# Kernel optimization log

Hardware: AMD Instinct MI355X
Metric: run time of the kernel (lower is better)

Reference implementation:

```python
import jax, jax.numpy as jnp
import numpy as np

N = 8192
F_IN = 128
F_OUT = 128
BLOCK = 64  # row block for the masked neighbor max-pool (keeps peak mem ~256MB)


def setup_inputs() -> dict:
    key = jax.random.key(0)
    k_in, k_adj, k_w, k_b = jax.random.split(key, 4)
    x = jax.random.normal(k_in, (N, F_IN), dtype=jnp.float32)
    adj = (jax.random.uniform(k_adj, (N, N)) < 0.01).astype(jnp.float32)
    adj = adj.at[jnp.arange(N), jnp.arange(N)].set(1.0)
    stdv = 1.0 / np.sqrt(F_OUT)
    weight = jax.random.uniform(k_w, (F_IN, F_OUT), minval=-stdv, maxval=stdv, dtype=jnp.float32)
    bias = jax.random.uniform(k_b, (F_OUT,), minval=-stdv, maxval=stdv, dtype=jnp.float32)
    return {"input": x, "adj": adj, "weight": weight, "bias": bias}


def _graph_pool(out, adj):
    # For each row i: max over features of out[j] where adj[i, j] != 0.
    # Blocked scan over rows to avoid materializing [N, N, F].
    neg = jnp.asarray(jnp.finfo(out.dtype).min, out.dtype)

    def body(_, adj_blk):  # adj_blk: [BLOCK, N]
        masked = jnp.where(adj_blk[:, :, None] != 0, out[None, :, :], neg)  # [BLOCK, N, F]
        return None, jnp.max(masked, axis=1)

    _, blocks = jax.lax.scan(body, None, adj.reshape(N // BLOCK, BLOCK, N))
    return blocks.reshape(N, out.shape[-1])


def reference(input, adj, weight, bias):
    h = input @ weight                       # [N, F_out]
    out = jnp.maximum(adj @ h + bias, 0.0)   # aggregate + bias + relu
    return _graph_pool(out, adj)             # per-node neighbor max-pool
```

## Files before the change

### kernel.cpp

```cpp
#include <hip/hip_runtime.h>
#include <float.h>

constexpr int N = 8192;
constexpr int F = 128;
constexpr int CAP = 256;

using short8 = __attribute__((ext_vector_type(8))) short;
using float4v = __attribute__((ext_vector_type(4))) float;

static __device__ inline unsigned short f2bf(float f) {
    unsigned u = __float_as_uint(f);
    u += 0x7fffu + ((u >> 16) & 1u);
    return (unsigned short)(u >> 16);
}
static __device__ inline float bf2f(unsigned short s) {
    return __uint_as_float((unsigned)s << 16);
}

constexpr int KP = 136;

__global__ __launch_bounds__(256) void gemm_mfma(const float* __restrict__ x,
                                                 const float* __restrict__ w,
                                                 unsigned short* __restrict__ h) {
    __shared__ unsigned short xs[64][KP];
    __shared__ unsigned short wt[128][KP];

    const int tid = threadIdx.x;
    const int row0 = blockIdx.x * 64;

    {
        const float4* x4 = (const float4*)(x + (size_t)row0 * F);
        #pragma unroll
        for (int i = tid; i < 64 * F / 4; i += 256) {
            const float4 v = x4[i];
            const int r = (i * 4) >> 7, c = (i * 4) & 127;
            xs[r][c + 0] = f2bf(v.x); xs[r][c + 1] = f2bf(v.y);
            xs[r][c + 2] = f2bf(v.z); xs[r][c + 3] = f2bf(v.w);
        }
    }
    {
        const float4* w4 = (const float4*)w;
        #pragma unroll
        for (int i = tid; i < F * F / 4; i += 256) {
            const float4 v = w4[i];
            const int k = (i * 4) >> 7, n = (i * 4) & 127;
            wt[n + 0][k] = f2bf(v.x); wt[n + 1][k] = f2bf(v.y);
            wt[n + 2][k] = f2bf(v.z); wt[n + 3][k] = f2bf(v.w);
        }
    }
    __syncthreads();

    const int lane = tid & 63, wid = tid >> 6;
    const int m = lane & 15, quad = lane >> 4;
    const int m0 = wid * 16;

    float4v acc[8];
    #pragma unroll
    for (int nt = 0; nt < 8; ++nt) acc[nt] = (float4v){0.f, 0.f, 0.f, 0.f};

    #pragma unroll
    for (int k0 = 0; k0 < F; k0 += 32) {
        const short8 a = *(const short8*)&xs[m0 + m][k0 + quad * 8];
        #pragma unroll
        for (int nt = 0; nt < 8; ++nt) {
            const short8 b = *(const short8*)&wt[nt * 16 + m][k0 + quad * 8];
            acc[nt] = __builtin_amdgcn_mfma_f32_16x16x32_bf16(a, b, acc[nt], 0, 0, 0);
        }
    }

    #pragma unroll
    for (int nt = 0; nt < 8; ++nt)
        #pragma unroll
        for (int r = 0; r < 4; ++r) {
            const int row = row0 + m0 + quad * 4 + r;
            const int col = nt * 16 + m;
            h[(size_t)row * F + col] = f2bf(acc[nt][r]);
        }
}

__global__ __launch_bounds__(256) void aggregate_relu_build_csr(
        const float* __restrict__ adj,
        const unsigned short* __restrict__ h,
        const float* __restrict__ bias,
        unsigned short* __restrict__ out2,
        unsigned short* __restrict__ csr_idx,
        int* __restrict__ csr_cnt) {
    __shared__ int idx[CAP];
    __shared__ int cnt;
    __shared__ float partial[F];

    const int tid  = threadIdx.x;
    const int lane = tid & 63;
    const int row  = blockIdx.x;

    if (tid == 0) cnt = 0;
    __syncthreads();

    const float4v* arow = (const float4v*)(adj + (size_t)row * N);
    float4v v[8];
    #pragma unroll
    for (int it = 0; it < 8; ++it) v[it] = __builtin_nontemporal_load(arow + tid + it * 256);

    const unsigned long long lt = (1ull << lane) - 1ull;
    #pragma unroll
    for (int it = 0; it < 8; ++it) {
        const int j4 = 4 * (tid + it * 256);
        const float4v vv = v[it];
        const unsigned long long m0 = __ballot(vv.x != 0.f);
        const unsigned long long m1 = __ballot(vv.y != 0.f);
        const unsigned long long m2 = __ballot(vv.z != 0.f);
        const unsigned long long m3 = __ballot(vv.w != 0.f);
        const int c0 = __popcll(m0), c1 = __popcll(m1),
                  c2 = __popcll(m2), c3 = __popcll(m3);
        const int tot = c0 + c1 + c2 + c3;
        int base = 0;
        if (lane == 0 && tot) base = atomicAdd(&cnt, tot);
        base = __shfl(base, 0, 64);
        if (vv.x != 0.f) idx[base + __popcll(m0 & lt)] = j4 + 0;
        base += c0;
        if (vv.y != 0.f) idx[base + __popcll(m1 & lt)] = j4 + 1;
        base += c1;
        if (vv.z != 0.f) idx[base + __popcll(m2 & lt)] = j4 + 2;
        base += c2;
        if (vv.w != 0.f) idx[base + __popcll(m3 & lt)] = j4 + 3;
    }
    __syncthreads();

    const int n = min(cnt, CAP);

    if (tid == 0) csr_cnt[row] = n;
    if (tid < n) csr_idx[(size_t)row * CAP + tid] = (unsigned short)idx[tid];

    const int f = tid & (F - 1);
    const int half = tid >> 7;

    float acc = 0.f;
    int e = half;
    for (; e + 6 < n; e += 8) {
        const int j0 = idx[e], j1 = idx[e + 2], j2 = idx[e + 4], j3 = idx[e + 6];
        const float a0 = bf2f(h[(size_t)j0 * F + f]);
        const float a1 = bf2f(h[(size_t)j1 * F + f]);
        const float a2 = bf2f(h[(size_t)j2 * F + f]);
        const float a3 = bf2f(h[(size_t)j3 * F + f]);
        acc += (a0 + a1) + (a2 + a3);
    }
    for (; e < n; e += 2) acc += bf2f(h[(size_t)idx[e] * F + f]);

    if (half == 1) partial[f] = acc;
    __syncthreads();
    if (half == 0) {
        acc += partial[f];
        const float vb = acc + bias[f];
        out2[(size_t)row * F + f] = f2bf(vb > 0.f ? vb : 0.f);
    }
}

__global__ __launch_bounds__(256) void neighbor_max_csr(
        const unsigned short* __restrict__ csr_idx,
        const int* __restrict__ csr_cnt,
        const unsigned short* __restrict__ out2,
        float* __restrict__ out) {
    __shared__ int idx[CAP];
    __shared__ float partial[F];

    const int tid = threadIdx.x;
    const int row = blockIdx.x;

    const int n = csr_cnt[row];
    if (tid < n) idx[tid] = csr_idx[(size_t)row * CAP + tid];
    __syncthreads();

    const int f = tid & (F - 1);
    const int half = tid >> 7;

    float acc = -FLT_MAX;
    int e = half;
    for (; e + 6 < n; e += 8) {
        const int j0 = idx[e], j1 = idx[e + 2], j2 = idx[e + 4], j3 = idx[e + 6];
        const float a0 = bf2f(out2[(size_t)j0 * F + f]);
        const float a1 = bf2f(out2[(size_t)j1 * F + f]);
        const float a2 = bf2f(out2[(size_t)j2 * F + f]);
        const float a3 = bf2f(out2[(size_t)j3 * F + f]);
        acc = fmaxf(acc, fmaxf(fmaxf(a0, a1), fmaxf(a2, a3)));
    }
    for (; e < n; e += 2) acc = fmaxf(acc, bf2f(out2[(size_t)idx[e] * F + f]));

    if (half == 1) partial[f] = acc;
    __syncthreads();
    if (half == 0) {
        acc = fmaxf(acc, partial[f]);
        out[(size_t)row * F + f] = acc;
    }
}

extern "C" void kernel_launch(void* const* d_in, const int* in_sizes, int n_in,
                              void* d_out, int out_size, void* d_ws, size_t ws_size,
                              hipStream_t stream) {
    const float* x    = (const float*)d_in[0];
    const float* adj  = (const float*)d_in[1];
    const float* w    = (const float*)d_in[2];
    const float* bias = (const float*)d_in[3];
    float* out = (float*)d_out;

    unsigned short* h    = (unsigned short*)d_ws;
    unsigned short* out2 = h + (size_t)N * F;
    int* csr_cnt = (int*)(out2 + (size_t)N * F);
    unsigned short* csr_idx = (unsigned short*)(csr_cnt + N);

    gemm_mfma<<<N / 64, 256, 0, stream>>>(x, w, h);
    aggregate_relu_build_csr<<<N, 256, 0, stream>>>(adj, h, bias, out2, csr_idx, csr_cnt);
    neighbor_max_csr<<<N, 256, 0, stream>>>(csr_idx, csr_cnt, out2, out);
}
```

Measured before the change: 386.5 us.

## Pack bf16 pairs per lane and split neighbor gathers across four wavefronts

The aggregate and max-pool kernels now have each lane load one 32-bit word holding two bf16 features. Each of the four wavefronts covers a full 128-feature row for every fourth neighbor, then partials are combined through shared memory. This halves the gather load instructions per neighbor and makes bias loads and output stores wider. The GEMM also uses 32-row tiles split into two column halves per wave, doubling the block count and halving accumulator registers, at the cost of reloading W per block. The dominant cost is still streaming the dense adjacency, so overall gains may be limited.

```diff
diff --git a/kernel.cpp b/kernel.cpp
--- a/kernel.cpp
+++ b/kernel.cpp
@@ -22,16 +22,16 @@
 __global__ __launch_bounds__(256) void gemm_mfma(const float* __restrict__ x,
                                                  const float* __restrict__ w,
                                                  unsigned short* __restrict__ h) {
-    __shared__ unsigned short xs[64][KP];
+    __shared__ unsigned short xs[32][KP];
     __shared__ unsigned short wt[128][KP];
 
     const int tid = threadIdx.x;
-    const int row0 = blockIdx.x * 64;
+    const int row0 = blockIdx.x * 32;
 
     {
         const float4* x4 = (const float4*)(x + (size_t)row0 * F);
         #pragma unroll
-        for (int i = tid; i < 64 * F / 4; i += 256) {
+        for (int i = tid; i < 32 * F / 4; i += 256) {
             const float4 v = x4[i];
             const int r = (i * 4) >> 7, c = (i * 4) & 127;
             xs[r][c + 0] = f2bf(v.x); xs[r][c + 1] = f2bf(v.y);
@@ -52,28 +52,29 @@
 
     const int lane = tid & 63, wid = tid >> 6;
     const int m = lane & 15, quad = lane >> 4;
-    const int m0 = wid * 16;
-
-    float4v acc[8];
-    #pragma unroll
-    for (int nt = 0; nt < 8; ++nt) acc[nt] = (float4v){0.f, 0.f, 0.f, 0.f};
+    const int m0 = (wid & 1) * 16;
+    const int nh = (wid >> 1) * 64;
+
+    float4v acc[4];
+    #pragma unroll
+    for (int nt = 0; nt < 4; ++nt) acc[nt] = (float4v){0.f, 0.f, 0.f, 0.f};
 
     #pragma unroll
     for (int k0 = 0; k0 < F; k0 += 32) {
         const short8 a = *(const short8*)&xs[m0 + m][k0 + quad * 8];
         #pragma unroll
-        for (int nt = 0; nt < 8; ++nt) {
-            const short8 b = *(const short8*)&wt[nt * 16 + m][k0 + quad * 8];
+        for (int nt = 0; nt < 4; ++nt) {
+            const short8 b = *(const short8*)&wt[nh + nt * 16 + m][k0 + quad * 8];
             acc[nt] = __builtin_amdgcn_mfma_f32_16x16x32_bf16(a, b, acc[nt], 0, 0, 0);
         }
     }
 
     #pragma unroll
-    for (int nt = 0; nt < 8; ++nt)
+    for (int nt = 0; nt < 4; ++nt)
         #pragma unroll
         for (int r = 0; r < 4; ++r) {
             const int row = row0 + m0 + quad * 4 + r;
-            const int col = nt * 16 + m;
+            const int col = nh + nt * 16 + m;
             h[(size_t)row * F + col] = f2bf(acc[nt][r]);
         }
 }
@@ -87,10 +88,11 @@
         int* __restrict__ csr_cnt) {
     __shared__ int idx[CAP];
     __shared__ int cnt;
-    __shared__ float partial[F];
+    __shared__ float2 p2[3][64];
 
     const int tid  = threadIdx.x;
     const int lane = tid & 63;
+    const int wv   = tid >> 6;
     const int row  = blockIdx.x;
 
     if (tid == 0) cnt = 0;
@@ -131,27 +133,36 @@
     if (tid == 0) csr_cnt[row] = n;
     if (tid < n) csr_idx[(size_t)row * CAP + tid] = (unsigned short)idx[tid];
 
-    const int f = tid & (F - 1);
-    const int half = tid >> 7;
-
-    float acc = 0.f;
-    int e = half;
-    for (; e + 6 < n; e += 8) {
-        const int j0 = idx[e], j1 = idx[e + 2], j2 = idx[e + 4], j3 = idx[e + 6];
-        const float a0 = bf2f(h[(size_t)j0 * F + f]);
-        const float a1 = bf2f(h[(size_t)j1 * F + f]);
-        const float a2 = bf2f(h[(size_t)j2 * F + f]);
-        const float a3 = bf2f(h[(size_t)j3 * F + f]);
-        acc += (a0 + a1) + (a2 + a3);
-    }
-    for (; e < n; e += 2) acc += bf2f(h[(size_t)idx[e] * F + f]);
-
-    if (half == 1) partial[f] = acc;
-    __syncthreads();
-    if (half == 0) {
-        acc += partial[f];
-        const float vb = acc + bias[f];
-        out2[(size_t)row * F + f] = f2bf(vb > 0.f ? vb : 0.f);
+    const unsigned* h32 = (const unsigned*)h;
+    float a0 = 0.f, a1 = 0.f;
+    int e = wv;
+    for (; e + 12 < n; e += 16) {
+        const unsigned u0 = h32[(size_t)idx[e]      * 64 + lane];
+        const unsigned u1 = h32[(size_t)idx[e + 4]  * 64 + lane];
+        const unsigned u2 = h32[(size_t)idx[e + 8]  * 64 + lane];
+        const unsigned u3 = h32[(size_t)idx[e + 12] * 64 + lane];
+        a0 += (bf2f((unsigned short)u0) + bf2f((unsigned short)u1))
+            + (bf2f((unsigned short)u2) + bf2f((unsigned short)u3));
+        a1 += (bf2f((unsigned short)(u0 >> 16)) + bf2f((unsigned short)(u1 >> 16)))
+            + (bf2f((unsigned short)(u2 >> 16)) + bf2f((unsigned short)(u3 >> 16)));
+    }
+    for (; e < n; e += 4) {
+        const unsigned u = h32[(size_t)idx[e] * 64 + lane];
+        a0 += bf2f((unsigned short)u);
+        a1 += bf2f((unsigned short)(u >> 16));
+    }
+
+    if (wv) p2[wv - 1][lane] = make_float2(a0, a1);
+    __syncthreads();
+    if (wv == 0) {
+        a0 += p2[0][lane].x + p2[1][lane].x + p2[2][lane].x;
+        a1 += p2[0][lane].y + p2[1][lane].y + p2[2][lane].y;
+        const float2 b2 = ((const float2*)bias)[lane];
+        float v0 = a0 + b2.x, v1 = a1 + b2.y;
+        v0 = v0 > 0.f ? v0 : 0.f;
+        v1 = v1 > 0.f ? v1 : 0.f;
+        ((unsigned*)out2)[(size_t)row * 64 + lane] =
+            (unsigned)f2bf(v0) | ((unsigned)f2bf(v1) << 16);
     }
 }
 
@@ -161,35 +172,42 @@
         const unsigned short* __restrict__ out2,
         float* __restrict__ out) {
     __shared__ int idx[CAP];
-    __shared__ float partial[F];
-
-    const int tid = threadIdx.x;
-    const int row = blockIdx.x;
+    __shared__ float2 p2[3][64];
+
+    const int tid  = threadIdx.x;
+    const int lane = tid & 63;
+    const int wv   = tid >> 6;
+    const int row  = blockIdx.x;
 
     const int n = csr_cnt[row];
     if (tid < n) idx[tid] = csr_idx[(size_t)row * CAP + tid];
     __syncthreads();
 
-    const int f = tid & (F - 1);
-    const int half = tid >> 7;
-
-    float acc = -FLT_MAX;
-    int e = half;
-    for (; e + 6 < n; e += 8) {
-        const int j0 = idx[e], j1 = idx[e + 2], j2 = idx[e + 4], j3 = idx[e + 6];
-        const float a0 = bf2f(out2[(size_t)j0 * F + f]);
-        const float a1 = bf2f(out2[(size_t)j1 * F + f]);
-        const float a2 = bf2f(out2[(size_t)j2 * F + f]);
-        const float a3 = bf2f(out2[(size_t)j3 * F + f]);
-        acc = fmaxf(acc, fmaxf(fmaxf(a0, a1), fmaxf(a2, a3)));
-    }
-    for (; e < n; e += 2) acc = fmaxf(acc, bf2f(out2[(size_t)idx[e] * F + f]));
-
-    if (half == 1) partial[f] = acc;
-    __syncthreads();
-    if (half == 0) {
-        acc = fmaxf(acc, partial[f]);
-        out[(size_t)row * F + f] = acc;
+    const unsigned* o32 = (const unsigned*)out2;
+    float a0 = -FLT_MAX, a1 = -FLT_MAX;
+    int e = wv;
+    for (; e + 12 < n; e += 16) {
+        const unsigned u0 = o32[(size_t)idx[e]      * 64 + lane];
+        const unsigned u1 = o32[(size_t)idx[e + 4]  * 64 + lane];
+        const unsigned u2 = o32[(size_t)idx[e + 8]  * 64 + lane];
+        const unsigned u3 = o32[(size_t)idx[e + 12] * 64 + lane];
+        a0 = fmaxf(a0, fmaxf(fmaxf(bf2f((unsigned short)u0), bf2f((unsigned short)u1)),
+                             fmaxf(bf2f((unsigned short)u2), bf2f((unsigned short)u3))));
+        a1 = fmaxf(a1, fmaxf(fmaxf(bf2f((unsigned short)(u0 >> 16)), bf2f((unsigned short)(u1 >> 16))),
+                             fmaxf(bf2f((unsigned short)(u2 >> 16)), bf2f((unsigned short)(u3 >> 16)))));
+    }
+    for (; e < n; e += 4) {
+        const unsigned u = o32[(size_t)idx[e] * 64 + lane];
+        a0 = fmaxf(a0, bf2f((unsigned short)u));
+        a1 = fmaxf(a1, bf2f((unsigned short)(u >> 16)));
+    }
+
+    if (wv) p2[wv - 1][lane] = make_float2(a0, a1);
+    __syncthreads();
+    if (wv == 0) {
+        a0 = fmaxf(a0, fmaxf(fmaxf(p2[0][lane].x, p2[1][lane].x), p2[2][lane].x));
+        a1 = fmaxf(a1, fmaxf(fmaxf(p2[0][lane].y, p2[1][lane].y), p2[2][lane].y));
+        ((float2*)out)[(size_t)row * 64 + lane] = make_float2(a0, a1);
     }
 }
 
@@ -207,7 +225,7 @@
     int* csr_cnt = (int*)(out2 + (size_t)N * F);
     unsigned short* csr_idx = (unsigned short*)(csr_cnt + N);
 
-    gemm_mfma<<<N / 64, 256, 0, stream>>>(x, w, h);
+    gemm_mfma<<<N / 32, 256, 0, stream>>>(x, w, h);
     aggregate_relu_build_csr<<<N, 256, 0, stream>>>(adj, h, bias, out2, csr_idx, csr_cnt);
     neighbor_max_csr<<<N, 256, 0, stream>>>(csr_idx, csr_cnt, out2, out);
 }
```

Result: faster. 374.6 us (-3.1%).
